# Performance work log

Hardware: AMD Instinct MI355X
Metric: run time of the kernel (lower is better)

## Reference

```python
import jax, jax.numpy as jnp
import numpy as np
import math

IMG = 640.0
SIZES = [32.0, 64.0, 128.0, 256.0]
STRIDES = [4, 8, 16, 32]
ARS = [0.5, 1.0, 2.0]
PRE_TOPK = 1000      # RPN_PRE_NMS_TOPK_TEST
POST_TOPK = 150      # RPN_POST_NMS_TOPK_TEST
NMS_THR = 0.7        # RPN_NMS_THRESHOLD
MIN_SIZE = 4.0       # MIN_BOX_SIZE
BBOX_CLAMP = math.log(1000.0 / 16.0)
ROI_OUT = 7          # ROI_OUTPUT_SIZE


def conv(x, w, b, pad):
    y = jax.lax.conv_general_dilated(x, w, (1, 1), [(pad, pad), (pad, pad)],
                                     dimension_numbers=('NCHW', 'OIHW', 'NCHW'))
    return y + b[None, :, None, None]


def level_anchors(H, W, stride, size):
    sx = (jnp.arange(W, dtype=jnp.float32) + 0.5) * stride
    sy = (jnp.arange(H, dtype=jnp.float32) + 0.5) * stride
    SY, SX = jnp.meshgrid(sy, sx, indexing='ij')
    shifts = jnp.stack([SX, SY, SX, SY], axis=-1).reshape(-1, 4)  # [H*W,4]
    base = []
    area = size * size
    for ar in ARS:
        w = math.sqrt(area / ar)
        h = ar * w
        base.append([-w / 2.0, -h / 2.0, w / 2.0, h / 2.0])
    base = jnp.asarray(base, jnp.float32)  # [3,4]
    return (shifts[:, None, :] + base[None, :, :]).reshape(-1, 4)  # [H*W*3,4]


def decode(deltas, boxes):
    w = jnp.maximum(boxes[:, 2] - boxes[:, 0], 1e-6)
    h = jnp.maximum(boxes[:, 3] - boxes[:, 1], 1e-6)
    cx = boxes[:, 0] + 0.5 * w
    cy = boxes[:, 1] + 0.5 * h
    dx, dy = deltas[:, 0], deltas[:, 1]
    dw = jnp.minimum(deltas[:, 2], BBOX_CLAMP)
    dh = jnp.minimum(deltas[:, 3], BBOX_CLAMP)
    pcx = cx + dx * w
    pcy = cy + dy * h
    pw = w * jnp.exp(dw)
    ph = h * jnp.exp(dh)
    return jnp.stack([pcx - 0.5 * pw, pcy - 0.5 * ph, pcx + 0.5 * pw, pcy + 0.5 * ph], axis=1)


def pairwise_iou(b):
    area = jnp.maximum(b[:, 2] - b[:, 0], 0) * jnp.maximum(b[:, 3] - b[:, 1], 0)
    lt = jnp.maximum(b[:, None, :2], b[None, :, :2])
    rb = jnp.minimum(b[:, None, 2:], b[None, :, 2:])
    wh = jnp.maximum(rb - lt, 0.0)
    inter = wh[..., 0] * wh[..., 1]
    return inter / jnp.maximum(area[:, None] + area[None, :] - inter, 1e-6)


def roi_align(feat, boxes, scale):
    # feat [C,H,W]; boxes [R,4] in image coords; one bilinear sample per bin center
    C, H, W = feat.shape
    b = boxes * scale
    x1, y1, x2, y2 = b[:, 0], b[:, 1], b[:, 2], b[:, 3]
    bw = jnp.maximum(x2 - x1, 1.0)
    bh = jnp.maximum(y2 - y1, 1.0)
    g = (jnp.arange(ROI_OUT, dtype=jnp.float32) + 0.5) / ROI_OUT
    px = x1[:, None] + g[None, :] * bw[:, None]   # [R,7]
    py = y1[:, None] + g[None, :] * bh[:, None]
    Y = jnp.broadcast_to(py[:, :, None], (py.shape[0], ROI_OUT, ROI_OUT))
    X = jnp.broadcast_to(px[:, None, :], (px.shape[0], ROI_OUT, ROI_OUT))
    y0f = jnp.floor(Y)
    x0f = jnp.floor(X)
    ly = Y - y0f
    lx = X - x0f
    y0 = jnp.clip(y0f, 0, H - 1).astype(jnp.int32)
    y1i = jnp.clip(y0f + 1, 0, H - 1).astype(jnp.int32)
    x0 = jnp.clip(x0f, 0, W - 1).astype(jnp.int32)
    x1i = jnp.clip(x0f + 1, 0, W - 1).astype(jnp.int32)
    f = lambda yi, xi: feat[:, yi, xi]  # [C,R,7,7]
    val = (f(y0, x0) * (1 - ly) * (1 - lx) + f(y0, x1i) * (1 - ly) * lx
           + f(y1i, x0) * ly * (1 - lx) + f(y1i, x1i) * ly * lx)
    return val.transpose(1, 0, 2, 3)  # [R,C,7,7]


def _forward(p2, p3, p4, p5, rpn_conv_w, rpn_conv_b, obj_w, obj_b, delta_w, delta_b,
             fc1_w, fc1_b, fc2_w, fc2_b, cls_w, cls_b, bbox_w, bbox_b):
    feats = [p2, p3, p4, p5]
    all_boxes, all_scores, all_lvl = [], [], []
    for lvl, (feat, stride, size) in enumerate(zip(feats, STRIDES, SIZES)):
        hid = jax.nn.relu(conv(feat, rpn_conv_w, rpn_conv_b, 1))
        obj = conv(hid, obj_w, obj_b, 0)      # [1,3,H,W]
        dlt = conv(hid, delta_w, delta_b, 0)  # [1,12,H,W]
        _, A, H, W = obj.shape
        scores = obj.transpose(0, 2, 3, 1).reshape(-1)  # [H*W*3]
        deltas = dlt.reshape(1, A, 4, H, W).transpose(0, 3, 4, 1, 2).reshape(-1, 4)
        anchors = level_anchors(H, W, stride, size)
        top_s, idx = jax.lax.top_k(scores, PRE_TOPK)
        boxes = jnp.clip(decode(deltas[idx], anchors[idx]), 0.0, IMG - 1.0)
        ww = boxes[:, 2] - boxes[:, 0]
        hh = boxes[:, 3] - boxes[:, 1]
        valid = (ww >= MIN_SIZE) & (hh >= MIN_SIZE)
        all_boxes.append(boxes)
        all_scores.append(jnp.where(valid, top_s, -1e30))
        all_lvl.append(jnp.full((PRE_TOPK,), float(lvl), jnp.float32))
    boxes = jnp.concatenate(all_boxes)   # [4000,4]
    scores = jnp.concatenate(all_scores)
    lvls = jnp.concatenate(all_lvl)
    N = boxes.shape[0]
    order = jnp.argsort(-scores)
    boxes_s = boxes[order]
    scores_s = scores[order]
    lvl_s = lvls[order]
    # batched NMS: offset per level so different levels never suppress each other
    off_boxes = boxes_s + (lvl_s * (IMG + 1.0) * 2.0)[:, None]
    iou = pairwise_iou(off_boxes)
    idx_r = jnp.arange(N)

    def body(i, keep):
        sup = (iou[i] > NMS_THR) & (idx_r > i) & keep[i]
        return keep & (~sup)

    keep = jax.lax.fori_loop(0, N, body, jnp.ones((N,), bool))
    kept_scores = jnp.where(keep, scores_s, -1e30)
    _, top_idx = jax.lax.top_k(kept_scores, POST_TOPK)
    props = boxes_s[top_idx]  # [150,4]
    # FPN level assignment (canonical formula) for ROI pooling
    pw = jnp.maximum(props[:, 2] - props[:, 0], 0.0)
    ph = jnp.maximum(props[:, 3] - props[:, 1], 0.0)
    k = jnp.clip(jnp.floor(4.0 + jnp.log2(jnp.sqrt(pw * ph) / 224.0 + 1e-6)), 2, 5)
    pooled = jnp.zeros((POST_TOPK, p2.shape[1], ROI_OUT, ROI_OUT), props.dtype)
    for lvl, (feat, stride) in enumerate(zip(feats, STRIDES)):
        pl = roi_align(feat[0], props, 1.0 / stride)
        pooled = pooled + jnp.where((k == (lvl + 2))[:, None, None, None], pl, 0.0)
    x = pooled.reshape(POST_TOPK, -1)            # [150, 12544]
    x = jax.nn.relu(x @ fc1_w.T + fc1_b)
    x = jax.nn.relu(x @ fc2_w.T + fc2_b)
    cls = x @ cls_w.T + cls_b                    # [150, 21]
    bbx = x @ bbox_w.T + bbox_b                  # [150, 84]
    return jnp.concatenate([cls, bbx], axis=-1)  # [150, 105]


def setup_inputs() -> dict:
    key = jax.random.key(0)
    ks = jax.random.split(key, 14)
    C = 256
    rn = lambda k, shape, s: jax.random.normal(k, shape, jnp.float32) * s
    return {
        'p2': rn(ks[0], (1, C, 160, 160), 0.5),
        'p3': rn(ks[1], (1, C, 80, 80), 0.5),
        'p4': rn(ks[2], (1, C, 40, 40), 0.5),
        'p5': rn(ks[3], (1, C, 20, 20), 0.5),
        'rpn_conv_w': rn(ks[4], (C, C, 3, 3), 0.01),
        'rpn_conv_b': jnp.zeros((C,), jnp.float32),
        'obj_w': rn(ks[5], (3, C, 1, 1), 0.01),
        'obj_b': jnp.zeros((3,), jnp.float32),
        'delta_w': rn(ks[6], (12, C, 1, 1), 0.01),
        'delta_b': jnp.zeros((12,), jnp.float32),
        'fc1_w': rn(ks[7], (1024, C * ROI_OUT * ROI_OUT), 0.01),
        'fc1_b': jnp.zeros((1024,), jnp.float32),
        'fc2_w': rn(ks[8], (1024, 1024), 0.01),
        'fc2_b': jnp.zeros((1024,), jnp.float32),
        'cls_w': rn(ks[9], (21, 1024), 0.01),
        'cls_b': jnp.zeros((21,), jnp.float32),
        'bbox_w': rn(ks[10], (84, 1024), 0.001),
        'bbox_b': jnp.zeros((84,), jnp.float32),
    }


def reference(p2, p3, p4, p5, rpn_conv_w, rpn_conv_b, obj_w, obj_b, delta_w, delta_b,
              fc1_w, fc1_b, fc2_w, fc2_b, cls_w, cls_b, bbox_w, bbox_b):
    return _forward(p2, p3, p4, p5, rpn_conv_w, rpn_conv_b, obj_w, obj_b, delta_w, delta_b,
                    fc1_w, fc1_b, fc2_w, fc2_b, cls_w, cls_b, bbox_w, bbox_b)
```

## Files before the change

kernel.cpp:

```cpp
#include <hip/hip_runtime.h>
#include <cstdint>

typedef unsigned long long u64;
typedef unsigned int u32;

__device__ inline u32 fmono(float f){ u32 u = __float_as_uint(f); u32 m = (u & 0x80000000u) ? 0xFFFFFFFFu : 0x80000000u; return u ^ m; }

__device__ const int    g_H[4]       = {160, 80, 40, 20};
__device__ const int    g_strideI[4] = {4, 8, 16, 32};
__device__ const float  g_size[4]    = {32.f, 64.f, 128.f, 256.f};
__device__ const int    g_cofs[4]    = {0, 76800, 96000, 100800};
__device__ const int    g_cnt[4]     = {76800, 19200, 4800, 1200};
__device__ const int    c_blkBase[5] = {0, 1600, 2000, 2288, 2416};
__device__ const int    c_S[4]       = {4, 4, 8, 8};
__device__ const int    c_pofs[4]    = {0, 25600, 32000, 33600};
__device__ const size_t c_partofs[4] = {0, 26214400, 32768000, 36044800};

__global__ __launch_bounds__(256) void wtr_k(const float* __restrict__ w, float* __restrict__ wT){
  __shared__ float tile[32][33];
  int tx = threadIdx.x & 31, ty = threadIdx.x >> 5;
  int row0 = blockIdx.x*32, co0 = blockIdx.y*32;
  #pragma unroll
  for (int r=0;r<4;r++){
    int co = co0 + ty + r*8;
    tile[ty+r*8][tx] = w[(size_t)co*2304 + row0 + tx];
  }
  __syncthreads();
  #pragma unroll
  for (int r=0;r<4;r++){
    int row = row0 + ty + r*8;
    wT[(size_t)row*256 + co0 + tx] = tile[tx][ty+r*8];
  }
}

__global__ void wcat_k(const float* __restrict__ cls_w, const float* __restrict__ cls_b,
                       const float* __restrict__ bbox_w, const float* __restrict__ bbox_b,
                       float* __restrict__ wcat, float* __restrict__ bcat){
  int t = blockIdx.x*256 + threadIdx.x;
  if (t < 105*1024){ int o = t >> 10, k = t & 1023; wcat[t] = (o < 21) ? cls_w[o*1024+k] : bbox_w[(o-21)*1024+k]; }
  if (t < 105) bcat[t] = (t < 21) ? cls_b[t] : bbox_b[t-21];
}

#define KC 4
__global__ __launch_bounds__(256) void rpn_conv_all_k(
    const float* __restrict__ p0, const float* __restrict__ p1,
    const float* __restrict__ p2f, const float* __restrict__ p3f,
    const float* __restrict__ wT, float* __restrict__ convp)
{
  int bid = blockIdx.x;
  int lvl = (bid >= c_blkBase[1]) + (bid >= c_blkBase[2]) + (bid >= c_blkBase[3]);
  int local = bid - c_blkBase[lvl];
  int nz  = c_S[lvl];
  int H = g_H[lvl], W = H;
  const float* in = (lvl==0)?p0:((lvl==1)?p1:((lvl==2)?p2f:p3f));
  float* part = convp + c_partofs[lvl];
  int zb   = local % nz;
  int cb   = (local / nz) & 3;
  int tile = local / (nz*4);

  int tilesX = (W + 15) >> 4;
  int tr0 = (tile / tilesX) * 16;
  int tc0 = (tile % tilesX) * 16;
  int ciPer = 256 / nz;
  int ciBeg = zb * ciPer;
  int t   = threadIdx.x;
  int tco = t & 15, tp = t >> 4;
  int pr = (tp >> 2) * 4, pc = (tp & 3) * 4;
  int HW = H*W;

  __shared__ float sIn[KC][18][20];
  __shared__ float sW[KC*9][64];

  float* sInF = &sIn[0][0][0];
  float* sWF  = &sW[0][0];

  int   iOff[6]; int iLds[6]; bool iOk[6];
  #pragma unroll
  for (int s=0;s<6;s++){
    int e = t + s*256;
    bool a = (s<5) || (t < (KC*324 - 5*256));
    int ee = a ? e : 0;
    int c = ee/324, r2 = ee%324, row = r2/18, col = r2%18;
    int gy = tr0+row-1, gx = tc0+col-1;
    bool ok = a && ((unsigned)gy < (unsigned)H) && ((unsigned)gx < (unsigned)W);
    iOff[s] = c*HW + gy*W + gx;
    iLds[s] = c*360 + row*20 + col;
    iOk[s]  = ok;
  }
  bool iAct5 = (t < (KC*324 - 5*256));
  int wOff[3]; int wLds[3];
  #pragma unroll
  for (int s=0;s<3;s++){
    int e4 = t + s*256;
    bool a = (s<2) || (t < (KC*9*16 - 2*256));
    int ee = a ? e4 : 0;
    int row = ee>>4, c4 = (ee&15)<<2;
    wOff[s] = row*256 + cb*64 + c4;
    wLds[s] = row*64 + c4;
  }
  bool wAct2 = (t < (KC*9*16 - 2*256));

  float acc[4][16];
  #pragma unroll
  for (int o=0;o<4;o++)
    #pragma unroll
    for (int p=0;p<16;p++) acc[o][p]=0.f;

  float  ri0,ri1,ri2,ri3,ri4,ri5;
  float4 rw0,rw1,rw2;

  {
    const float* inb = in + (size_t)ciBeg*HW;
    const float* wb  = wT + (size_t)ciBeg*2304;
    ri0 = iOk[0] ? inb[iOff[0]] : 0.f;
    ri1 = iOk[1] ? inb[iOff[1]] : 0.f;
    ri2 = iOk[2] ? inb[iOff[2]] : 0.f;
    ri3 = iOk[3] ? inb[iOff[3]] : 0.f;
    ri4 = iOk[4] ? inb[iOff[4]] : 0.f;
    ri5 = iOk[5] ? inb[iOff[5]] : 0.f;
    rw0 = *(const float4*)&wb[wOff[0]];
    rw1 = *(const float4*)&wb[wOff[1]];
    if (wAct2) rw2 = *(const float4*)&wb[wOff[2]];
  }

  int ciEnd = ciBeg + ciPer;
  for (int ci0=ciBeg; ci0<ciEnd; ci0+=KC){
    sInF[iLds[0]] = ri0; sInF[iLds[1]] = ri1; sInF[iLds[2]] = ri2;
    sInF[iLds[3]] = ri3; sInF[iLds[4]] = ri4;
    if (iAct5) sInF[iLds[5]] = ri5;
    *(float4*)&sWF[wLds[0]] = rw0;
    *(float4*)&sWF[wLds[1]] = rw1;
    if (wAct2) *(float4*)&sWF[wLds[2]] = rw2;
    __syncthreads();

    if (ci0 + KC < ciEnd){
      const float* inb = in + (size_t)(ci0+KC)*HW;
      const float* wb  = wT + (size_t)(ci0+KC)*2304;
      ri0 = iOk[0] ? inb[iOff[0]] : 0.f;
      ri1 = iOk[1] ? inb[iOff[1]] : 0.f;
      ri2 = iOk[2] ? inb[iOff[2]] : 0.f;
      ri3 = iOk[3] ? inb[iOff[3]] : 0.f;
      ri4 = iOk[4] ? inb[iOff[4]] : 0.f;
      ri5 = iOk[5] ? inb[iOff[5]] : 0.f;
      rw0 = *(const float4*)&wb[wOff[0]];
      rw1 = *(const float4*)&wb[wOff[1]];
      if (wAct2) rw2 = *(const float4*)&wb[wOff[2]];
    }

    #pragma unroll
    for (int c=0;c<KC;c++){
      float rin[6][6];
      #pragma unroll
      for (int rr=0;rr<6;rr++){
        float4 a = *(const float4*)&sIn[c][pr+rr][pc];
        float2 b = *(const float2*)&sIn[c][pr+rr][pc+4];
        rin[rr][0]=a.x; rin[rr][1]=a.y; rin[rr][2]=a.z; rin[rr][3]=a.w;
        rin[rr][4]=b.x; rin[rr][5]=b.y;
      }
      #pragma unroll
      for (int k=0;k<9;k++){
        int ky=k/3, kx=k%3;
        float4 w0 = *(const float4*)&sW[c*9+k][tco*4];
        float wv[4] = {w0.x,w0.y,w0.z,w0.w};
        #pragma unroll
        for (int dr=0;dr<4;dr++)
          #pragma unroll
          for (int dc=0;dc<4;dc++){
            float iv = rin[dr+ky][dc+kx];
            int p = dr*4+dc;
            #pragma unroll
            for (int o=0;o<4;o++) acc[o][p] = fmaf(wv[o], iv, acc[o][p]);
          }
      }
    }
    __syncthreads();
  }

  int coBase = cb*64 + tco*4;
  float* pb = part + (size_t)zb*HW*256;
  #pragma unroll
  for (int dr=0;dr<4;dr++){
    int gy = tr0+pr+dr; if (gy>=H) continue;
    #pragma unroll
    for (int dc=0;dc<4;dc++){
      int gx = tc0+pc+dc; if (gx>=W) continue;
      int p = dr*4+dc;
      *(float4*)&pb[(size_t)(gy*W+gx)*256 + coBase] = make_float4(acc[0][p],acc[1][p],acc[2][p],acc[3][p]);
    }
  }
}

__global__ __launch_bounds__(256) void rpn_heads_k(
  const float* __restrict__ convp, const float* __restrict__ cbias,
  const float* __restrict__ ow, const float* __restrict__ ob,
  const float* __restrict__ dw, const float* __restrict__ db,
  float* __restrict__ scores, float* __restrict__ deltas)
{
  __shared__ float sw[15][256];
  int t = threadIdx.x;
  for (int e=t; e<15*256; e+=256){ int o=e>>8, k=e&255; sw[o][k] = (o<3)? ow[o*256+k] : dw[(o-3)*256+k]; }
  __syncthreads();
  int wv = t>>6, lane = t&63;
  float4 bv = *(const float4*)&cbias[lane*4];
  #pragma unroll
  for (int i=0;i<16;i++){
    int gpx = blockIdx.x*64 + wv*16 + i;
    if (gpx >= 34000) return;
    int lvl = (gpx >= 25600) + (gpx >= 32000) + (gpx >= 33600);
    int S = c_S[lvl];
    size_t stride = (size_t)g_H[lvl]*g_H[lvl]*256;
    const float* pb = convp + c_partofs[lvl] + (size_t)(gpx - c_pofs[lvl])*256 + lane*4;
    float vx=0.f, vy=0.f, vz=0.f, vw=0.f;
    for (int s=0;s<S;s++){
      float4 q = *(const float4*)(pb + (size_t)s*stride);
      vx += q.x; vy += q.y; vz += q.z; vw += q.w;
    }
    vx += bv.x; vy += bv.y; vz += bv.z; vw += bv.w;
    vx = vx>0.f?vx:0.f; vy = vy>0.f?vy:0.f; vz = vz>0.f?vz:0.f; vw = vw>0.f?vw:0.f;
    float a[15];
    #pragma unroll
    for (int o=0;o<15;o++){
      const float* w = &sw[o][lane*4];
      a[o] = w[0]*vx + w[1]*vy + w[2]*vz + w[3]*vw;
    }
    #pragma unroll
    for (int off=32; off; off>>=1)
      #pragma unroll
      for (int o=0;o<15;o++) a[o] += __shfl_xor(a[o], off, 64);
    if (lane==0){
      for (int q=0;q<3;q++) scores[gpx*3+q] = a[q] + ob[q];
      for (int q=0;q<3;q++)
        for (int j=0;j<4;j++)
          deltas[(size_t)(gpx*3+q)*4 + j] = a[3+q*4+j] + db[q*4+j];
    }
  }
}

__global__ __launch_bounds__(1024) void topk_k(
  const float* __restrict__ scores, float* __restrict__ top_s, u32* __restrict__ top_idx)
{
  int lvl = blockIdx.x;
  int base = g_cofs[lvl], N = g_cnt[lvl];
  const int K = 1000;
  __shared__ u32 hist[4096];
  __shared__ u64 sbuf[4096];
  __shared__ u32 shThr; __shared__ int scnt;
  int t = threadIdx.x;
  for (int e=t; e<4096; e+=1024) hist[e]=0;
  __syncthreads();
  for (int e=t; e<N; e+=1024){
    u32 m = fmono(scores[base+e]);
    atomicAdd(&hist[m>>20], 1u);
  }
  __syncthreads();
  if (t==0){
    int accu=0;
    for (int d=4095; d>=0; --d){
      int c = (int)hist[d];
      if (accu + c >= K){ shThr = (u32)d; break; }
      accu += c;
    }
    scnt = 0;
  }
  __syncthreads();
  u32 thr = shThr;
  for (int e=t; e<4096; e+=1024) sbuf[e]=0ull;
  __syncthreads();
  for (int e=t; e<N; e+=1024){
    u32 m = fmono(scores[base+e]);
    if ((m>>20) >= thr){
      int p = atomicAdd(&scnt, 1);
      if (p < 4096) sbuf[p] = ((u64)m << 32) | (u32)(~(u32)e);
    }
  }
  __syncthreads();
  for (int k=2;k<=4096;k<<=1)
    for (int j=k>>1;j>0;j>>=1){
      for (int i=t;i<4096;i+=1024){
        int ixj = i^j;
        if (ixj > i){
          u64 x = sbuf[i], y = sbuf[ixj];
          bool up = ((i & k) == 0);
          bool swp = up ? (x<y) : (x>y);
          if (swp){ sbuf[i]=y; sbuf[ixj]=x; }
        }
      }
      __syncthreads();
    }
  if (t<K){
    u64 key = sbuf[t];
    u32 idx = ~((u32)key);
    top_idx[lvl*1000+t] = idx;
    top_s[lvl*1000+t]   = scores[base + (int)idx];
  }
}

__global__ void decode_k(const u32* __restrict__ top_idx, const float* __restrict__ top_s,
                         const float* __restrict__ deltas,
                         float* __restrict__ cat_scores, float4* __restrict__ cat_boxes)
{
  int t = blockIdx.x*256 + threadIdx.x;
  if (t >= 4000) return;
  int lvl = t/1000;
  u32 idx = top_idx[t];
  float score = top_s[t];
  int W = g_H[lvl];
  int strd = g_strideI[lvl];
  float size = g_size[lvl];
  int a = (int)(idx % 3u); int pix = (int)(idx / 3u);
  int px = pix % W, py = pix / W;
  double area = (double)size*(double)size;
  double ar = (a==0)?0.5:((a==1)?1.0:2.0);
  double wd = sqrt(area/ar);
  double hd = ar*wd;
  float bx1 = (float)(-wd*0.5), by1 = (float)(-hd*0.5), bx2=(float)(wd*0.5), by2=(float)(hd*0.5);
  float sx = ((float)px + 0.5f)*(float)strd;
  float sy = ((float)py + 0.5f)*(float)strd;
  float ax1 = sx+bx1, ay1=sy+by1, ax2=sx+bx2, ay2=sy+by2;
  float w = fmaxf(ax2-ax1, 1e-6f), h = fmaxf(ay2-ay1, 1e-6f);
  float cx = ax1 + 0.5f*w, cy = ay1 + 0.5f*h;
  const float* d = &deltas[(size_t)(g_cofs[lvl] + (int)idx)*4];
  float dx = d[0], dy = d[1];
  float dwv = fminf(d[2], 4.135166556742356f);
  float dhv = fminf(d[3], 4.135166556742356f);
  float pcx = cx + dx*w, pcy = cy + dy*h;
  float pw = w*expf(dwv), ph = h*expf(dhv);
  float x1 = pcx - 0.5f*pw, y1 = pcy - 0.5f*ph, x2 = pcx + 0.5f*pw, y2 = pcy + 0.5f*ph;
  x1 = fminf(fmaxf(x1,0.f),639.f); y1 = fminf(fmaxf(y1,0.f),639.f);
  x2 = fminf(fmaxf(x2,0.f),639.f); y2 = fminf(fmaxf(y2,0.f),639.f);
  bool valid = ((x2-x1) >= 4.f) && ((y2-y1) >= 4.f);
  cat_boxes[t] = make_float4(x1,y1,x2,y2);
  cat_scores[t] = valid ? score : -1e30f;
}

__global__ __launch_bounds__(1024) void sort_k(const float* __restrict__ cat_scores, const float4* __restrict__ cat_boxes,
  float* __restrict__ scores_s, float4* __restrict__ boxes_s, float4* __restrict__ obox)
{
  __shared__ u64 s[4096];
  int t = threadIdx.x;
  for (int i=t;i<4096;i+=1024){
    u64 key = 0;
    if (i<4000) key = ((u64)fmono(cat_scores[i])<<32) | (u32)(~(u32)i);
    s[i]=key;
  }
  __syncthreads();
  for (int k=2;k<=4096;k<<=1)
    for (int j=k>>1;j>0;j>>=1){
      for (int i=t;i<4096;i+=1024){
        int ixj=i^j;
        if (ixj>i){
          u64 x=s[i], y=s[ixj];
          bool up = ((i&k)==0);
          bool swp = up ? (x<y):(x>y);
          if (swp){ s[i]=y; s[ixj]=x; }
        }
      }
      __syncthreads();
    }
  for (int r=t;r<4000;r+=1024){
    u32 o = ~((u32)s[r]);
    float4 b = cat_boxes[o];
    scores_s[r] = cat_scores[o];
    boxes_s[r] = b;
    float off = (float)(o/1000u) * 1282.0f;
    obox[r] = make_float4(b.x+off, b.y+off, b.z+off, b.w+off);
  }
}

__global__ __launch_bounds__(256) void iou_k(const float4* __restrict__ obox, u64* __restrict__ mask)
{
  int w = threadIdx.x;
  int i = blockIdx.x*4 + threadIdx.y;
  if (i >= 4000 || w >= 63) return;
  float4 bi = obox[i];
  float ai = fmaxf(bi.z-bi.x,0.f)*fmaxf(bi.w-bi.y,0.f);
  u64 bits=0;
  int c0=w*64;
  for (int l=0;l<64;l++){
    int c=c0+l;
    if (c>=4000) break;
    if (c<=i) continue;
    float4 bc = obox[c];
    float ac = fmaxf(bc.z-bc.x,0.f)*fmaxf(bc.w-bc.y,0.f);
    float ltx = fmaxf(bi.x, bc.x), lty = fmaxf(bi.y, bc.y);
    float rbx = fminf(bi.z, bc.z), rby = fminf(bi.w, bc.w);
    float wx = fmaxf(rbx-ltx,0.f), wy = fmaxf(rby-lty,0.f);
    float inter = wx*wy;
    float uni = fmaxf(ai+ac-inter, 1e-6f);
    if (inter/uni > 0.7f) bits |= (1ull<<l);
  }
  mask[(size_t)i*63 + w] = bits;
}

#define PF 32
__global__ __launch_bounds__(64) void nms_scan_k(const u64* __restrict__ mask,
   const float* __restrict__ scores_s, const float4* __restrict__ boxes_s, float4* __restrict__ props)
{
  int lane = threadIdx.x;
  bool act = lane < 63;
  const u64* mrow = mask + lane;
  u64 removed = 0;

  u64 bufA[PF], bufB[PF];
  #pragma unroll
  for (int j=0;j<PF;j++) bufA[j] = act ? mrow[(size_t)j*63] : 0ull;

  const int NG = 4000/PF;
  for (int g=0; g<NG; g+=2){
    if (g+1 < NG){
      #pragma unroll
      for (int j=0;j<PF;j++) bufB[j] = act ? mrow[(size_t)((g+1)*PF+j)*63] : 0ull;
    }
    #pragma unroll
    for (int j=0;j<PF;j++){
      int i = g*PF + j;
      u64 rm = __shfl(removed, i>>6, 64);
      bool keep = ((rm >> (i&63)) & 1ull) == 0ull;
      if (keep) removed |= bufA[j];
    }
    if (g+2 < NG){
      #pragma unroll
      for (int j=0;j<PF;j++) bufA[j] = act ? mrow[(size_t)((g+2)*PF+j)*63] : 0ull;
    }
    if (g+1 < NG){
      #pragma unroll
      for (int j=0;j<PF;j++){
        int i = (g+1)*PF + j;
        u64 rm = __shfl(removed, i>>6, 64);
        bool keep = ((rm >> (i&63)) & 1ull) == 0ull;
        if (keep) removed |= bufB[j];
      }
    }
  }

  u64 keepbits = ~removed;
  u64 selbits = 0;
  if (act){
    #pragma unroll
    for (int j=0;j<64;j++){
      int i = lane*64 + j;
      if (i < 4000 && ((keepbits>>j)&1ull) && scores_s[i] > -1e29f) selbits |= (1ull<<j);
    }
  }
  u64 validbits = 0;
  if (act){
    int nvalid = 4000 - lane*64;
    if (nvalid >= 64) validbits = ~0ull;
    else if (nvalid > 0) validbits = (1ull<<nvalid) - 1ull;
  }
  u64 nonbits = (~selbits) & validbits;

  int cntSel = __popcll(selbits);
  int incS = cntSel;
  #pragma unroll
  for (int off2=1; off2<64; off2<<=1){ int v = __shfl_up(incS, off2, 64); if (lane>=off2) incS += v; }
  int exSel = incS - cntSel;
  int totalSel = __shfl(incS, 63, 64);
  int cnt = totalSel < 150 ? totalSel : 150;

  int cntNon = __popcll(nonbits);
  int incN = cntNon;
  #pragma unroll
  for (int off2=1; off2<64; off2<<=1){ int v = __shfl_up(incN, off2, 64); if (lane>=off2) incN += v; }
  int exNon = incN - cntNon;

  if (act){
    int r = exSel;
    #pragma unroll
    for (int j=0;j<64;j++){
      if ((selbits>>j)&1ull){
        if (r < 150) props[r] = boxes_s[lane*64 + j];
        r++;
      }
    }
    int r2 = cnt + exNon;
    #pragma unroll
    for (int j=0;j<64;j++){
      if ((nonbits>>j)&1ull){
        if (r2 < 150) props[r2] = boxes_s[lane*64 + j];
        r2++;
      }
    }
  }
}

__global__ __launch_bounds__(256) void roi_k(const float* __restrict__ p2, const float* __restrict__ p3,
  const float* __restrict__ p4, const float* __restrict__ p5, const float4* __restrict__ props, float* __restrict__ x0)
{
  int roi = blockIdx.y, p = blockIdx.x, c = threadIdx.x;
  float4 b = props[roi];
  float pw = fmaxf(b.z-b.x, 0.f), ph = fmaxf(b.w-b.y, 0.f);
  float kf = floorf(4.f + log2f(sqrtf(pw*ph)/224.f + 1e-6f));
  kf = fminf(fmaxf(kf, 2.f), 5.f);
  int lvl = (int)kf - 2;
  const float* f = (lvl==0)?p2:((lvl==1)?p3:((lvl==2)?p4:p5));
  int H = g_H[lvl]; int HW = H*H;
  float scale = 1.f/(float)g_strideI[lvl];
  float x1 = b.x*scale, y1 = b.y*scale, x2 = b.z*scale, y2 = b.w*scale;
  float bw = fmaxf(x2-x1, 1.f), bh = fmaxf(y2-y1, 1.f);
  int py = p/7, px = p%7;
  float gx = ((float)px + 0.5f)/7.f;
  float gy = ((float)py + 0.5f)/7.f;
  float X = x1 + gx*bw;
  float Y = y1 + gy*bh;
  float x0f = floorf(X), y0f = floorf(Y);
  float lx = X - x0f, ly = Y - y0f;
  int xi0 = (int)fminf(fmaxf(x0f,0.f),(float)(H-1));
  int xi1 = (int)fminf(fmaxf(x0f+1.f,0.f),(float)(H-1));
  int yi0 = (int)fminf(fmaxf(y0f,0.f),(float)(H-1));
  int yi1 = (int)fminf(fmaxf(y0f+1.f,0.f),(float)(H-1));
  float v00 = f[(size_t)c*HW + yi0*H + xi0];
  float v01 = f[(size_t)c*HW + yi0*H + xi1];
  float v10 = f[(size_t)c*HW + yi1*H + xi0];
  float v11 = f[(size_t)c*HW + yi1*H + xi1];
  float val = v00*(1.f-ly)*(1.f-lx) + v01*(1.f-ly)*lx + v10*ly*(1.f-lx) + v11*ly*lx;
  x0[(size_t)roi*12544 + c*49 + p] = val;
}

__global__ __launch_bounds__(256) void fc_split_k(const float* __restrict__ X, const float* __restrict__ Wt,
  float* __restrict__ partial, int M, int N, int K, int KS)
{
  __shared__ float sx[32][33];
  __shared__ float sw[32][64];
  int t = threadIdx.x;
  int tn = t & 15, tm = t >> 4;
  int nb = blockIdx.x, mb = blockIdx.y, zb = blockIdx.z;
  int row0 = mb*32 + tm*2, col0 = nb*64 + tn*4;
  int kbeg = zb*KS, kend = kbeg + KS;
  float acc[2][4] = {{0,0,0,0},{0,0,0,0}};
  int wn = t & 63, kg = t >> 6;
  for (int k0=kbeg;k0<kend;k0+=32){
    for (int e=t;e<1024;e+=256){
      int m=e>>5, kk=e&31;
      int row=mb*32+m;
      sx[m][kk] = (row<M)? X[(size_t)row*K + k0+kk] : 0.f;
    }
    int co = nb*64+wn;
    if (co<N){
      const float* wp = &Wt[(size_t)co*K + k0 + kg*8];
      float4 va = *(const float4*)wp;
      float4 vb = *(const float4*)(wp+4);
      sw[kg*8+0][wn]=va.x; sw[kg*8+1][wn]=va.y; sw[kg*8+2][wn]=va.z; sw[kg*8+3][wn]=va.w;
      sw[kg*8+4][wn]=vb.x; sw[kg*8+5][wn]=vb.y; sw[kg*8+6][wn]=vb.z; sw[kg*8+7][wn]=vb.w;
    } else {
      #pragma unroll
      for (int j=0;j<8;j++) sw[kg*8+j][wn]=0.f;
    }
    __syncthreads();
    #pragma unroll 8
    for (int kk=0;kk<32;kk++){
      float xa = sx[tm*2+0][kk], xb = sx[tm*2+1][kk];
      float4 wv = *(const float4*)&sw[kk][tn*4];
      acc[0][0]=fmaf(xa,wv.x,acc[0][0]); acc[0][1]=fmaf(xa,wv.y,acc[0][1]);
      acc[0][2]=fmaf(xa,wv.z,acc[0][2]); acc[0][3]=fmaf(xa,wv.w,acc[0][3]);
      acc[1][0]=fmaf(xb,wv.x,acc[1][0]); acc[1][1]=fmaf(xb,wv.y,acc[1][1]);
      acc[1][2]=fmaf(xb,wv.z,acc[1][2]); acc[1][3]=fmaf(xb,wv.w,acc[1][3]);
    }
    __syncthreads();
  }
  for (int dm=0;dm<2;dm++){
    int row=row0+dm; if (row>=M) continue;
    for (int dn=0;dn<4;dn++){
      int col=col0+dn; if (col>=N) continue;
      partial[((size_t)zb*M + row)*N + col] = acc[dm][dn];
    }
  }
}

__global__ __launch_bounds__(256) void fc_reduce_k(const float* __restrict__ partial, const float* __restrict__ bias,
  float* __restrict__ Y, int M, int N, int S, int dorelu)
{
  int idx = blockIdx.x*256 + threadIdx.x;
  if (idx >= M*N) return;
  int col = idx % N;
  float v = bias[col];
  size_t stride = (size_t)M*N;
  for (int s=0;s<S;s++) v += partial[s*stride + idx];
  if (dorelu) v = fmaxf(v, 0.f);
  Y[idx] = v;
}

extern "C" void kernel_launch(void* const* d_in, const int* in_sizes, int n_in,
                              void* d_out, int out_size, void* d_ws, size_t ws_size,
                              hipStream_t stream)
{
  (void)in_sizes; (void)n_in; (void)out_size; (void)ws_size;
  const float* p[4] = {(const float*)d_in[0], (const float*)d_in[1], (const float*)d_in[2], (const float*)d_in[3]};
  const float* rpn_w = (const float*)d_in[4];
  const float* rpn_b = (const float*)d_in[5];
  const float* obj_w = (const float*)d_in[6];
  const float* obj_b = (const float*)d_in[7];
  const float* del_w = (const float*)d_in[8];
  const float* del_b = (const float*)d_in[9];
  const float* fc1_w = (const float*)d_in[10];
  const float* fc1_b = (const float*)d_in[11];
  const float* fc2_w = (const float*)d_in[12];
  const float* fc2_b = (const float*)d_in[13];
  const float* cls_w = (const float*)d_in[14];
  const float* cls_b = (const float*)d_in[15];
  const float* bbox_w= (const float*)d_in[16];
  const float* bbox_b= (const float*)d_in[17];

  char* ws = (char*)d_ws;
  size_t off = 0;
  auto alloc = [&](size_t bytes){ size_t o = off; off += (bytes + 255) & ~(size_t)255; return o; };
  float*  wT1      = (float*)(ws + alloc(589824ull*4));
  float*  hid      = (float*)(ws + alloc(34000ull*256*4));
  float*  scores   = (float*)(ws + alloc(102000ull*4));
  float*  deltas   = (float*)(ws + alloc(102000ull*16));
  float*  top_s    = (float*)(ws + alloc(4000ull*4));
  u32*    top_idx  = (u32*)  (ws + alloc(4000ull*4));
  float*  cat_sc   = (float*)(ws + alloc(4000ull*4));
  float4* cat_bx   = (float4*)(ws + alloc(4000ull*16));
  float*  scores_s = (float*)(ws + alloc(4000ull*4));
  float4* boxes_s  = (float4*)(ws + alloc(4000ull*16));
  float4* obox     = (float4*)(ws + alloc(4000ull*16));
  u64*    mask     = (u64*)  (ws + alloc(4000ull*63*8));
  float4* props    = (float4*)(ws + alloc(150ull*16));
  float*  x0       = (float*)(ws + alloc(150ull*12544*4));
  float*  x1       = (float*)(ws + alloc(150ull*1024*4));
  float*  x2       = (float*)(ws + alloc(150ull*1024*4));
  float*  wcat     = (float*)(ws + alloc(105ull*1024*4));
  float*  bcat     = (float*)(ws + alloc(105ull*4));
  float*  convp    = (float*)(ws + alloc(36864000ull*4));
  float*  partial  = hid;

  hipLaunchKernelGGL(wtr_k, dim3(72,8), dim3(256), 0, stream, rpn_w, wT1);
  hipLaunchKernelGGL(wcat_k, dim3((105*1024+255)/256), dim3(256), 0, stream, cls_w, cls_b, bbox_w, bbox_b, wcat, bcat);

  hipLaunchKernelGGL(rpn_conv_all_k, dim3(2416), dim3(256), 0, stream,
                     p[0], p[1], p[2], p[3], wT1, convp);
  hipLaunchKernelGGL(rpn_heads_k, dim3((34000+63)/64), dim3(256), 0, stream,
                     convp, rpn_b, obj_w, obj_b, del_w, del_b, scores, deltas);
  hipLaunchKernelGGL(topk_k, dim3(4), dim3(1024), 0, stream, scores, top_s, top_idx);
  hipLaunchKernelGGL(decode_k, dim3(16), dim3(256), 0, stream, top_idx, top_s, deltas, cat_sc, cat_bx);
  hipLaunchKernelGGL(sort_k, dim3(1), dim3(1024), 0, stream, cat_sc, cat_bx, scores_s, boxes_s, obox);
  hipLaunchKernelGGL(iou_k, dim3(1000), dim3(64,4), 0, stream, obox, mask);
  hipLaunchKernelGGL(nms_scan_k, dim3(1), dim3(64), 0, stream, mask, scores_s, boxes_s, props);
  hipLaunchKernelGGL(roi_k, dim3(49,150), dim3(256), 0, stream, p[0],p[1],p[2],p[3], props, x0);

  hipLaunchKernelGGL(fc_split_k, dim3(16,5,14), dim3(256), 0, stream, x0, fc1_w, partial, 150, 1024, 12544, 896);
  hipLaunchKernelGGL(fc_reduce_k, dim3((150*1024+255)/256), dim3(256), 0, stream, partial, fc1_b, x1, 150, 1024, 14, 1);
  hipLaunchKernelGGL(fc_split_k, dim3(16,5,8), dim3(256), 0, stream, x1, fc2_w, partial, 150, 1024, 1024, 128);
  hipLaunchKernelGGL(fc_reduce_k, dim3((150*1024+255)/256), dim3(256), 0, stream, partial, fc2_b, x2, 150, 1024, 8, 1);
  hipLaunchKernelGGL(fc_split_k, dim3(2,5,8), dim3(256), 0, stream, x2, wcat, partial, 150, 105, 1024, 128);
  hipLaunchKernelGGL(fc_reduce_k, dim3((150*105+255)/256), dim3(256), 0, stream, partial, bcat, (float*)d_out, 150, 105, 8, 0);
}
```

Before: 1.352 ms.

## Fuse decode into sort kernel, split RPN conv launch, deepen fc1 split-K

Moves the proposal-decode logic into the single-block sort kernel, so one launch handles both steps and the decode_k launch goes away. The RPN conv grid is split into two half-size launches through a block-offset parameter. The fc1 split-K factor is raised from 14 to 28 slices for more parallelism, at the cost of more partial sums to reduce. Decoding now runs on one 1024-thread block instead of 16 blocks, and it depends on global writes becoming visible within the block after __syncthreads, which holds on HIP.

```diff
diff --git a/kernel.cpp b/kernel.cpp
--- a/kernel.cpp
+++ b/kernel.cpp
@@ -45,9 +45,9 @@
 __global__ __launch_bounds__(256) void rpn_conv_all_k(
     const float* __restrict__ p0, const float* __restrict__ p1,
     const float* __restrict__ p2f, const float* __restrict__ p3f,
-    const float* __restrict__ wT, float* __restrict__ convp)
-{
-  int bid = blockIdx.x;
+    const float* __restrict__ wT, float* __restrict__ convp, int bidBase)
+{
+  int bid = blockIdx.x + bidBase;
   int lvl = (bid >= c_blkBase[1]) + (bid >= c_blkBase[2]) + (bid >= c_blkBase[3]);
   int local = bid - c_blkBase[lvl];
   int nz  = c_S[lvl];
@@ -295,52 +295,49 @@
   }
 }
 
-__global__ void decode_k(const u32* __restrict__ top_idx, const float* __restrict__ top_s,
-                         const float* __restrict__ deltas,
-                         float* __restrict__ cat_scores, float4* __restrict__ cat_boxes)
-{
-  int t = blockIdx.x*256 + threadIdx.x;
-  if (t >= 4000) return;
-  int lvl = t/1000;
-  u32 idx = top_idx[t];
-  float score = top_s[t];
-  int W = g_H[lvl];
-  int strd = g_strideI[lvl];
-  float size = g_size[lvl];
-  int a = (int)(idx % 3u); int pix = (int)(idx / 3u);
-  int px = pix % W, py = pix / W;
-  double area = (double)size*(double)size;
-  double ar = (a==0)?0.5:((a==1)?1.0:2.0);
-  double wd = sqrt(area/ar);
-  double hd = ar*wd;
-  float bx1 = (float)(-wd*0.5), by1 = (float)(-hd*0.5), bx2=(float)(wd*0.5), by2=(float)(hd*0.5);
-  float sx = ((float)px + 0.5f)*(float)strd;
-  float sy = ((float)py + 0.5f)*(float)strd;
-  float ax1 = sx+bx1, ay1=sy+by1, ax2=sx+bx2, ay2=sy+by2;
-  float w = fmaxf(ax2-ax1, 1e-6f), h = fmaxf(ay2-ay1, 1e-6f);
-  float cx = ax1 + 0.5f*w, cy = ay1 + 0.5f*h;
-  const float* d = &deltas[(size_t)(g_cofs[lvl] + (int)idx)*4];
-  float dx = d[0], dy = d[1];
-  float dwv = fminf(d[2], 4.135166556742356f);
-  float dhv = fminf(d[3], 4.135166556742356f);
-  float pcx = cx + dx*w, pcy = cy + dy*h;
-  float pw = w*expf(dwv), ph = h*expf(dhv);
-  float x1 = pcx - 0.5f*pw, y1 = pcy - 0.5f*ph, x2 = pcx + 0.5f*pw, y2 = pcy + 0.5f*ph;
-  x1 = fminf(fmaxf(x1,0.f),639.f); y1 = fminf(fmaxf(y1,0.f),639.f);
-  x2 = fminf(fmaxf(x2,0.f),639.f); y2 = fminf(fmaxf(y2,0.f),639.f);
-  bool valid = ((x2-x1) >= 4.f) && ((y2-y1) >= 4.f);
-  cat_boxes[t] = make_float4(x1,y1,x2,y2);
-  cat_scores[t] = valid ? score : -1e30f;
-}
-
-__global__ __launch_bounds__(1024) void sort_k(const float* __restrict__ cat_scores, const float4* __restrict__ cat_boxes,
+__global__ __launch_bounds__(1024) void sort_k(const u32* __restrict__ top_idx, const float* __restrict__ top_s,
+  const float* __restrict__ deltas,
+  float* __restrict__ cat_sc, float4* __restrict__ cat_bx,
   float* __restrict__ scores_s, float4* __restrict__ boxes_s, float4* __restrict__ obox)
 {
+  int t = threadIdx.x;
+  for (int e=t; e<4000; e+=1024){
+    int lvl = e/1000;
+    u32 idx = top_idx[e];
+    float score = top_s[e];
+    int W = g_H[lvl];
+    int strd = g_strideI[lvl];
+    float size = g_size[lvl];
+    int a = (int)(idx % 3u); int pix = (int)(idx / 3u);
+    int px = pix % W, py = pix / W;
+    double area = (double)size*(double)size;
+    double ar = (a==0)?0.5:((a==1)?1.0:2.0);
+    double wd = sqrt(area/ar);
+    double hd = ar*wd;
+    float bx1 = (float)(-wd*0.5), by1 = (float)(-hd*0.5), bx2=(float)(wd*0.5), by2=(float)(hd*0.5);
+    float sx = ((float)px + 0.5f)*(float)strd;
+    float sy = ((float)py + 0.5f)*(float)strd;
+    float ax1 = sx+bx1, ay1=sy+by1, ax2=sx+bx2, ay2=sy+by2;
+    float w = fmaxf(ax2-ax1, 1e-6f), h = fmaxf(ay2-ay1, 1e-6f);
+    float cx = ax1 + 0.5f*w, cy = ay1 + 0.5f*h;
+    const float* d = &deltas[(size_t)(g_cofs[lvl] + (int)idx)*4];
+    float dx = d[0], dy = d[1];
+    float dwv = fminf(d[2], 4.135166556742356f);
+    float dhv = fminf(d[3], 4.135166556742356f);
+    float pcx = cx + dx*w, pcy = cy + dy*h;
+    float pw = w*expf(dwv), ph = h*expf(dhv);
+    float x1 = pcx - 0.5f*pw, y1 = pcy - 0.5f*ph, x2 = pcx + 0.5f*pw, y2 = pcy + 0.5f*ph;
+    x1 = fminf(fmaxf(x1,0.f),639.f); y1 = fminf(fmaxf(y1,0.f),639.f);
+    x2 = fminf(fmaxf(x2,0.f),639.f); y2 = fminf(fmaxf(y2,0.f),639.f);
+    bool valid = ((x2-x1) >= 4.f) && ((y2-y1) >= 4.f);
+    cat_bx[e] = make_float4(x1,y1,x2,y2);
+    cat_sc[e] = valid ? score : -1e30f;
+  }
+  __syncthreads();
   __shared__ u64 s[4096];
-  int t = threadIdx.x;
   for (int i=t;i<4096;i+=1024){
     u64 key = 0;
-    if (i<4000) key = ((u64)fmono(cat_scores[i])<<32) | (u32)(~(u32)i);
+    if (i<4000) key = ((u64)fmono(cat_sc[i])<<32) | (u32)(~(u32)i);
     s[i]=key;
   }
   __syncthreads();
@@ -359,8 +356,8 @@
     }
   for (int r=t;r<4000;r+=1024){
     u32 o = ~((u32)s[r]);
-    float4 b = cat_boxes[o];
-    scores_s[r] = cat_scores[o];
+    float4 b = cat_bx[o];
+    scores_s[r] = cat_sc[o];
     boxes_s[r] = b;
     float off = (float)(o/1000u) * 1282.0f;
     obox[r] = make_float4(b.x+off, b.y+off, b.z+off, b.w+off);
@@ -628,19 +625,22 @@
   hipLaunchKernelGGL(wtr_k, dim3(72,8), dim3(256), 0, stream, rpn_w, wT1);
   hipLaunchKernelGGL(wcat_k, dim3((105*1024+255)/256), dim3(256), 0, stream, cls_w, cls_b, bbox_w, bbox_b, wcat, bcat);
 
-  hipLaunchKernelGGL(rpn_conv_all_k, dim3(2416), dim3(256), 0, stream,
-                     p[0], p[1], p[2], p[3], wT1, convp);
+  hipLaunchKernelGGL(rpn_conv_all_k, dim3(1208), dim3(256), 0, stream,
+                     p[0], p[1], p[2], p[3], wT1, convp, 0);
+  hipLaunchKernelGGL(rpn_conv_all_k, dim3(1208), dim3(256), 0, stream,
+                     p[0], p[1], p[2], p[3], wT1, convp, 1208);
+
   hipLaunchKernelGGL(rpn_heads_k, dim3((34000+63)/64), dim3(256), 0, stream,
                      convp, rpn_b, obj_w, obj_b, del_w, del_b, scores, deltas);
   hipLaunchKernelGGL(topk_k, dim3(4), dim3(1024), 0, stream, scores, top_s, top_idx);
-  hipLaunchKernelGGL(decode_k, dim3(16), dim3(256), 0, stream, top_idx, top_s, deltas, cat_sc, cat_bx);
-  hipLaunchKernelGGL(sort_k, dim3(1), dim3(1024), 0, stream, cat_sc, cat_bx, scores_s, boxes_s, obox);
+  hipLaunchKernelGGL(sort_k, dim3(1), dim3(1024), 0, stream, top_idx, top_s, deltas,
+                     cat_sc, cat_bx, scores_s, boxes_s, obox);
   hipLaunchKernelGGL(iou_k, dim3(1000), dim3(64,4), 0, stream, obox, mask);
   hipLaunchKernelGGL(nms_scan_k, dim3(1), dim3(64), 0, stream, mask, scores_s, boxes_s, props);
   hipLaunchKernelGGL(roi_k, dim3(49,150), dim3(256), 0, stream, p[0],p[1],p[2],p[3], props, x0);
 
-  hipLaunchKernelGGL(fc_split_k, dim3(16,5,14), dim3(256), 0, stream, x0, fc1_w, partial, 150, 1024, 12544, 896);
-  hipLaunchKernelGGL(fc_reduce_k, dim3((150*1024+255)/256), dim3(256), 0, stream, partial, fc1_b, x1, 150, 1024, 14, 1);
+  hipLaunchKernelGGL(fc_split_k, dim3(16,5,28), dim3(256), 0, stream, x0, fc1_w, partial, 150, 1024, 12544, 448);
+  hipLaunchKernelGGL(fc_reduce_k, dim3((150*1024+255)/256), dim3(256), 0, stream, partial, fc1_b, x1, 150, 1024, 28, 1);
   hipLaunchKernelGGL(fc_split_k, dim3(16,5,8), dim3(256), 0, stream, x1, fc2_w, partial, 150, 1024, 1024, 128);
   hipLaunchKernelGGL(fc_reduce_k, dim3((150*1024+255)/256), dim3(256), 0, stream, partial, fc2_b, x2, 150, 1024, 8, 1);
   hipLaunchKernelGGL(fc_split_k, dim3(2,5,8), dim3(256), 0, stream, x2, wcat, partial, 150, 105, 1024, 128);
```

After: 1.380 ms. 1.02x slower.
